# Kernel optimization log

Hardware: AMD Instinct MI355X
Metric: run time of the kernel (lower is better)

The kernel has to match this reference:

```python
import jax, jax.numpy as jnp
import numpy as np

N_ENT = 50000
N_REL = 16
D_E = 64
D_R = 64
D_OUT = 32
N_EDGE = 1000000


def setup_inputs() -> dict:
    key = jax.random.key(0)
    ks = jax.random.split(key, 8)
    # 0.1 scale keeps tanh / softmax in a realistic (non-saturated) range,
    # mimicking trained embedding magnitudes.
    entity_table = jax.random.normal(ks[0], (N_ENT, D_E), dtype=jnp.float32) * 0.1
    relation_table = jax.random.normal(ks[1], (N_REL, D_R), dtype=jnp.float32) * 0.1
    W_R = jax.random.normal(ks[2], (N_REL, D_E, D_R), dtype=jnp.float32) * (1.0 / np.sqrt(D_E))
    W1 = jax.random.normal(ks[3], (D_E, D_OUT), dtype=jnp.float32) * (1.0 / np.sqrt(D_E))
    b1 = jnp.zeros((D_OUT,), dtype=jnp.float32)
    W2 = jax.random.normal(ks[4], (D_E, D_OUT), dtype=jnp.float32) * (1.0 / np.sqrt(D_E))
    b2 = jnp.zeros((D_OUT,), dtype=jnp.float32)
    src = jax.random.randint(ks[5], (N_EDGE,), 0, N_ENT, dtype=jnp.int32)
    dst = jax.random.randint(ks[6], (N_EDGE,), 0, N_ENT, dtype=jnp.int32)
    etype = jax.random.randint(ks[7], (N_EDGE,), 0, N_REL, dtype=jnp.int32)
    return {"entity_table": entity_table, "relation_table": relation_table,
            "W_R": W_R, "W1": W1, "b1": b1, "W2": W2, "b2": b2,
            "src": src, "dst": dst, "etype": etype}


def reference(entity_table, relation_table, W_R, W1, b1, W2, b2, src, dst, etype):
    """KGAT calc_att (per-relation edge attention + edge softmax) followed by
    one bi-interaction Aggregator layer (dropout = identity, eval mode)."""
    n_nodes = entity_table.shape[0]
    # Per-relation projection of all node embeddings (grouped GEMM form of the
    # per-relation loop in compute_attention): [R, N, d_r]
    proj = jnp.einsum('nd,rde->rne', entity_table, W_R)
    r_mul_h = proj[etype, src]            # [E, d_r]  h W_r per edge
    r_mul_t = proj[etype, dst]            # [E, d_r]  t W_r per edge
    r_e = relation_table[etype]           # [E, d_r]
    # att = (h W_r) . tanh(t W_r + r)
    att = jnp.sum(r_mul_h * jnp.tanh(r_mul_t + r_e), axis=-1)  # [E]
    # edge softmax grouped by destination node
    att_max = jax.ops.segment_max(att, dst, num_segments=n_nodes)     # [N]
    ex = jnp.exp(att - att_max[dst])
    denom = jax.ops.segment_sum(ex, dst, num_segments=n_nodes)        # [N]
    a = ex / denom[dst]                                               # [E]
    # u_mul_e + sum: N_h[v] = sum_{(u->v)} a_e * node[u]
    msg = a[:, None] * entity_table[src]                              # [E, d]
    N_h = jax.ops.segment_sum(msg, dst, num_segments=n_nodes)         # [N, d]
    node = entity_table
    # bi-interaction aggregator (LeakyReLU slope 0.01, torch default)
    out1 = jax.nn.leaky_relu((node + N_h) @ W1 + b1)
    out2 = jax.nn.leaky_relu((node * N_h) @ W2 + b2)
    return out1 + out2
```

## Files before the change

kernel.cpp:

```cpp
#include <hip/hip_runtime.h>
#include <math.h>

#define NREL 16
#define DE 64
#define DOUT 32
#define NPART 16
#define TQ 392

typedef __attribute__((ext_vector_type(8))) short bf16x8;
typedef __attribute__((ext_vector_type(16))) float f32x16;
typedef __attribute__((ext_vector_type(2))) float f32x2;

__device__ __forceinline__ short f2bf(float f) {
    unsigned u = __builtin_bit_cast(unsigned, f);
    unsigned r = (u + 0x7FFFu + ((u >> 16) & 1u)) >> 16;
    return (short)r;
}
__device__ __forceinline__ unsigned char f2fp8(float f) {
    int p = __builtin_amdgcn_cvt_pk_fp8_f32(f, f, 0, false);
    return (unsigned char)(p & 0xff);
}
__device__ __forceinline__ float tanh_fast(float x) {
    float e = __expf(2.0f * x);
    return fmaf(-2.0f, __builtin_amdgcn_rcpf(e + 1.0f), 1.0f);
}
__device__ __forceinline__ void fp8x8_to_f32(uint2 u, float* f) {
    f32x2 a0 = __builtin_amdgcn_cvt_pk_f32_fp8(u.x, false);
    f32x2 a1 = __builtin_amdgcn_cvt_pk_f32_fp8(u.x, true);
    f32x2 a2 = __builtin_amdgcn_cvt_pk_f32_fp8(u.y, false);
    f32x2 a3 = __builtin_amdgcn_cvt_pk_f32_fp8(u.y, true);
    f[0] = a0[0]; f[1] = a0[1]; f[2] = a1[0]; f[3] = a1[1];
    f[4] = a2[0]; f[5] = a2[1]; f[6] = a3[0]; f[7] = a3[1];
}

__global__ __launch_bounds__(256) void prep_kernel(const float* __restrict__ ent,
                                                   short* __restrict__ entbf,
                                                   unsigned char* __restrict__ entf8,
                                                   int eTot,
                                                   const float* __restrict__ WR,
                                                   short* __restrict__ Wbf,
                                                   short* __restrict__ WTbf,
                                                   const int* __restrict__ dst,
                                                   int* __restrict__ counts,
                                                   int E, int psz,
                                                   int eB, int wB) {
    int b = blockIdx.x;
    if (b < eB) {
        int i = b * 256 + threadIdx.x;
        if (i < eTot) {
            float f = ent[i];
            entbf[i] = f2bf(f);
            entf8[i] = f2fp8(f);
        }
    } else if (b < eB + wB) {
        int i = (b - eB) * 256 + threadIdx.x;
        int r = i >> 12, k = (i >> 6) & 63, j = i & 63;
        short w = f2bf(WR[i]);
        Wbf[i] = w;
        WTbf[(r << 12) + (j << 6) + k] = w;
    } else {
        int hb = b - eB - wB;
        int part = hb & (NPART - 1);
        int i = (hb / NPART) * 256 + threadIdx.x;
        if (i < E) {
            int d = dst[i];
            if (d >= part * psz && d < (part + 1) * psz)
                atomicAdd(&counts[d], 1);
        }
    }
}

__global__ __launch_bounds__(256) void blocksum_kernel(const int* __restrict__ counts,
                                                       int* __restrict__ blockSums, int n) {
    __shared__ int wsum[4];
    int i = blockIdx.x * 256 + threadIdx.x;
    int v = (i < n) ? counts[i] : 0;
#pragma unroll
    for (int off = 1; off < 64; off <<= 1) v += __shfl_xor(v, off);
    if ((threadIdx.x & 63) == 0) wsum[threadIdx.x >> 6] = v;
    __syncthreads();
    if (threadIdx.x == 0)
        blockSums[blockIdx.x] = wsum[0] + wsum[1] + wsum[2] + wsum[3];
}

__global__ __launch_bounds__(1024) void blockscan_kernel(int* __restrict__ blockSums, int nb) {
    __shared__ int lds[1024];
    int t = threadIdx.x;
    int v = (t < nb) ? blockSums[t] : 0;
    lds[t] = v;
    __syncthreads();
    for (int off = 1; off < 1024; off <<= 1) {
        int u = (t >= off) ? lds[t - off] : 0;
        __syncthreads();
        lds[t] += u;
        __syncthreads();
    }
    if (t < nb) blockSums[t] = (t == 0) ? 0 : lds[t - 1];
}

__global__ __launch_bounds__(256) void scanout_kernel(const int* __restrict__ counts,
                                                      const int* __restrict__ blockSums,
                                                      int* __restrict__ offsets,
                                                      int* __restrict__ cursor, int n) {
    __shared__ int wsum[4];
    int t = threadIdx.x;
    int i = blockIdx.x * 256 + t;
    int lane = t & 63;
    int w = t >> 6;
    int v = (i < n) ? counts[i] : 0;
    int incl = v;
#pragma unroll
    for (int off = 1; off < 64; off <<= 1) {
        int u = __shfl_up(incl, off);
        if (lane >= off) incl += u;
    }
    if (lane == 63) wsum[w] = incl;
    __syncthreads();
    int woff = 0;
#pragma unroll
    for (int j = 0; j < 4; ++j) if (j < w) woff += wsum[j];
    int excl = incl - v + woff + blockSums[blockIdx.x];
    if (i < n) { offsets[i] = excl; cursor[i] = excl; }
    if (i == n - 1) offsets[n] = excl + v;
}

__global__ __launch_bounds__(256) void scatter_kernel(const int* __restrict__ dst,
                                                      const int* __restrict__ src,
                                                      const int* __restrict__ etype,
                                                      int* __restrict__ cursor,
                                                      int* __restrict__ pks,
                                                      int E, int psz) {
    int part = blockIdx.x & (NPART - 1);
    int i = (blockIdx.x / NPART) * 256 + threadIdx.x;
    if (i < E) {
        int d = dst[i];
        if (d >= part * psz && d < (part + 1) * psz) {
            int pos = atomicAdd(&cursor[d], 1);
            pks[pos] = (src[i] << 4) | etype[i];
        }
    }
}

__global__ __launch_bounds__(256) void projq_kernel(const short* __restrict__ entbf,
                                                    const float* __restrict__ rel,
                                                    const short* __restrict__ Wbf,
                                                    const short* __restrict__ WTbf,
                                                    unsigned char* __restrict__ Qf8,
                                                    int N) {
    __shared__ short Tl[4 * 2048];
    int lane = threadIdx.x & 63;
    int wid = threadIdx.x >> 6;
    int lin = blockIdx.x;
    int r = lin / TQ;
    int tq = lin - r * TQ;
    int m0 = (tq * 4 + wid) * 32;
    if (m0 >= N) return;
    int hi = lane >> 5;
    int lo = lane & 31;

    int arow = m0 + lo;
    if (arow >= N) arow = N - 1;
    const short* ap = entbf + ((size_t)arow << 6) + hi * 8;
    bf16x8 A[4];
#pragma unroll
    for (int kk = 0; kk < 4; ++kk) A[kk] = *(const bf16x8*)(ap + kk * 16);

    short* tb = Tl + wid * 2048;
    const short* wtb = WTbf + ((size_t)r << 12);
    const short* wb  = Wbf  + ((size_t)r << 12);

    f32x16 acc0 = {}, acc1 = {};
#pragma unroll
    for (int kk = 0; kk < 4; ++kk) {
        bf16x8 b0 = *(const bf16x8*)(wtb + lo * DE + kk * 16 + hi * 8);
        bf16x8 b1 = *(const bf16x8*)(wtb + (lo + 32) * DE + kk * 16 + hi * 8);
        acc0 = __builtin_amdgcn_mfma_f32_32x32x16_bf16(A[kk], b0, acc0, 0, 0, 0);
        acc1 = __builtin_amdgcn_mfma_f32_32x32x16_bf16(A[kk], b1, acc1, 0, 0, 0);
    }
    float rv0 = rel[r * DE + lo];
    float rv1 = rel[r * DE + 32 + lo];
#pragma unroll
    for (int i = 0; i < 16; ++i) {
        int row = (i & 3) + 8 * (i >> 2) + 4 * hi;
        int sw = (row & 7) << 3;
        tb[(row * DE + lo) ^ sw] = f2bf(tanh_fast(acc0[i] + rv0));
        tb[(row * DE + 32 + lo) ^ sw] = f2bf(tanh_fast(acc1[i] + rv1));
    }
    bf16x8 A2[4];
#pragma unroll
    for (int kk = 0; kk < 4; ++kk)
        A2[kk] = *(const bf16x8*)(tb + ((lo * DE + kk * 16 + hi * 8) ^ ((lo & 7) << 3)));

    f32x16 q0 = {}, q1 = {};
#pragma unroll
    for (int kk = 0; kk < 4; ++kk) {
        bf16x8 b0 = *(const bf16x8*)(wb + lo * DE + kk * 16 + hi * 8);
        bf16x8 b1 = *(const bf16x8*)(wb + (lo + 32) * DE + kk * 16 + hi * 8);
        q0 = __builtin_amdgcn_mfma_f32_32x32x16_bf16(A2[kk], b0, q0, 0, 0, 0);
        q1 = __builtin_amdgcn_mfma_f32_32x32x16_bf16(A2[kk], b1, q1, 0, 0, 0);
    }
    unsigned char* tb8 = (unsigned char*)tb;
#pragma unroll
    for (int i = 0; i < 16; ++i) {
        int row = (i & 3) + 8 * (i >> 2) + 4 * hi;
        tb8[row * DE + lo] = f2fp8(q0[i]);
        tb8[row * DE + 32 + lo] = f2fp8(q1[i]);
    }
#pragma unroll
    for (int p = 0; p < 4; ++p) {
        int row = p * 8 + (lane >> 3);
        int node = m0 + row;
        unsigned long long vq = *(const unsigned long long*)(tb8 + row * DE + (lane & 7) * 8);
        if (node < N)
            *(unsigned long long*)(Qf8 + (((size_t)r * N + node) << 6) + (lane & 7) * 8) = vq;
    }
}

__global__ __launch_bounds__(256) void agg_kernel(const float* __restrict__ ent,
                                                  const unsigned char* __restrict__ entf8,
                                                  const unsigned char* __restrict__ Qf8,
                                                  const int* __restrict__ offsets,
                                                  const int* __restrict__ pks,
                                                  const float* __restrict__ W1,
                                                  const float* __restrict__ b1,
                                                  const float* __restrict__ W2,
                                                  const float* __restrict__ b2,
                                                  float* __restrict__ out, int n) {
    __shared__ float xl[4][128];
    __shared__ unsigned char ql[4][NREL * DE];
    int lane = threadIdx.x & 63;
    int wid = threadIdx.x >> 6;
    int v = (blockIdx.x << 2) + wid;
    if (v >= n) return;
    int o0 = offsets[v], o1 = offsets[v + 1];
    int g = lane >> 3, gl = lane & 7;

    unsigned char* qw = &ql[wid][0];
#pragma unroll
    for (int pass = 0; pass < 4; ++pass) {
        int r = pass * 4 + (lane >> 4);
        int j4 = (lane & 15) * 4;
        unsigned qj = *(const unsigned*)(Qf8 + (((size_t)r * (unsigned)n + (unsigned)v) << 6) + j4);
        *(unsigned*)(&qw[(r << 6) + j4]) = qj;
    }

    float l = 0.f;
    float acc[8];
#pragma unroll
    for (int j = 0; j < 8; ++j) acc[j] = 0.f;

    int k0 = o0 + g;
    bool vv0 = k0 < o1;
    int pk0 = vv0 ? pks[k0] : 0;
    uint2 x0 = {};
    if (vv0) x0 = *(const uint2*)(entf8 + ((size_t)(pk0 >> 4) << 6) + gl * 8);
    int k1 = k0 + 8;
    bool vv1 = k1 < o1;
    int pk1 = vv1 ? pks[k1] : 0;
    uint2 x1 = {};
    if (vv1) x1 = *(const uint2*)(entf8 + ((size_t)(pk1 >> 4) << 6) + gl * 8);
    int k2 = k1 + 8;
    bool vv2 = k2 < o1;
    int pk2 = vv2 ? pks[k2] : 0;

    int iters = (o1 - o0 + 7) >> 3;
    for (int it = 0; it < iters; ++it) {
        uint2 x2 = {};
        if (vv2) x2 = *(const uint2*)(entf8 + ((size_t)(pk2 >> 4) << 6) + gl * 8);
        int k3 = k2 + 8;
        bool vv3 = k3 < o1;
        int pk3 = vv3 ? pks[k3] : 0;

        int rcur = pk0 & 15;
        uint2 qv = *(const uint2*)(&qw[(rcur << 6) + gl * 8]);
        float xf[8], qf[8];
        fp8x8_to_f32(x0, xf);
        fp8x8_to_f32(qv, qf);
        float d = 0.f;
#pragma unroll
        for (int j = 0; j < 8; ++j) d = fmaf(xf[j], qf[j], d);
        d += __shfl_xor(d, 1);
        d += __shfl_xor(d, 2);
        d += __shfl_xor(d, 4);
        float pe = vv0 ? __expf(d) : 0.f;
        l += pe;
#pragma unroll
        for (int j = 0; j < 8; ++j) acc[j] = fmaf(pe, xf[j], acc[j]);
        vv0 = vv1; x0 = x1; pk0 = pk1;
        vv1 = vv2; x1 = x2; pk1 = pk2;
        vv2 = vv3; pk2 = pk3; k2 = k3;
    }
#pragma unroll
    for (int off = 8; off < 64; off <<= 1) {
        l += __shfl_xor(l, off);
#pragma unroll
        for (int j = 0; j < 8; ++j) acc[j] += __shfl_xor(acc[j], off);
    }
    float* xw = &xl[wid][0];
    float invl = (l > 0.f) ? (1.0f / l) : 0.f;
    if (g == 0) {
#pragma unroll
        for (int j = 0; j < 8; ++j) xw[gl * 8 + j] = acc[j] * invl;
    }
    float node = ent[((size_t)v << 6) + lane];
    float Nh = xw[lane];
    float x1e = node + Nh;
    float x2e = node * Nh;
    xw[lane] = x1e;
    xw[64 + lane] = x2e;
    int j = lane & 31;
    const float* __restrict__ Wsel = (lane < 32) ? W1 : W2;
    float bias = (lane < 32) ? b1[j] : b2[j];
    const float* xb2 = xw + ((lane < 32) ? 0 : 64);
    float o = 0.f;
#pragma unroll 8
    for (int kk = 0; kk < DE; ++kk)
        o = fmaf(xb2[kk], Wsel[kk * DOUT + j], o);
    o += bias;
    float lr = (o > 0.f) ? o : 0.01f * o;
    float other = __shfl_xor(lr, 32);
    if (lane < 32) out[(size_t)v * DOUT + lane] = lr + other;
}

extern "C" void kernel_launch(void* const* d_in, const int* in_sizes, int n_in,
                              void* d_out, int out_size, void* d_ws, size_t ws_size,
                              hipStream_t stream) {
    const float* ent = (const float*)d_in[0];
    const float* rel = (const float*)d_in[1];
    const float* WR  = (const float*)d_in[2];
    const float* W1  = (const float*)d_in[3];
    const float* b1  = (const float*)d_in[4];
    const float* W2  = (const float*)d_in[5];
    const float* b2  = (const float*)d_in[6];
    const int* src   = (const int*)d_in[7];
    const int* dst   = (const int*)d_in[8];
    const int* ety   = (const int*)d_in[9];
    float* out       = (float*)d_out;

    const int E = in_sizes[7];
    const int N = in_sizes[0] / DE;
    const int NB = (N + 255) / 256;
    const int psz = (N + NPART - 1) / NPART;
    const int chunks = (E + 255) / 256;

    size_t qBytes  = (size_t)N * NREL * DE;
    size_t eElems  = (size_t)N * DE;
    size_t wElems  = (size_t)NREL * DE * DE;

    char* ws = (char*)d_ws;
    unsigned char* Qf8 = (unsigned char*)ws;
    short* entbf = (short*)(ws + qBytes);
    short* Wbf   = entbf + eElems;
    short* WTbf  = Wbf + wElems;
    unsigned char* entf8 = (unsigned char*)(WTbf + wElems);
    int* counts  = (int*)(entf8 + eElems);
    int* offsets = counts + N;
    int* cursor  = offsets + N + 1;
    int* pks     = cursor + N;
    int* bsums   = pks + E;
    size_t need  = (size_t)((char*)(bsums + NB) - ws);
    if (ws_size < need) return;

    const int eB = (int)((eElems + 255) / 256);
    const int wB = (int)(wElems / 256);

    hipMemsetAsync(counts, 0, (size_t)N * 4, stream);
    prep_kernel<<<eB + wB + chunks * NPART, 256, 0, stream>>>(
        ent, entbf, entf8, (int)eElems, WR, Wbf, WTbf, dst, counts, E, psz, eB, wB);
    blocksum_kernel<<<NB, 256, 0, stream>>>(counts, bsums, N);
    blockscan_kernel<<<1, 1024, 0, stream>>>(bsums, NB);
    scanout_kernel<<<NB, 256, 0, stream>>>(counts, bsums, offsets, cursor, N);
    scatter_kernel<<<chunks * NPART, 256, 0, stream>>>(dst, src, ety, cursor, pks, E, psz);
    projq_kernel<<<TQ * NREL, 256, 0, stream>>>(entbf, rel, Wbf, WTbf, Qf8, N);
    agg_kernel<<<(N + 3) / 4, 256, 0, stream>>>(ent, entf8, Qf8, offsets, pks,
                                                W1, b1, W2, b2, out, N);
}
```

Before: 227.9 us.

## Fuse per-relation projection into aggregation kernel via shared-memory Q tile

Merges the projection kernel and the aggregation kernel into one. Each block computes Q for its 32 destination nodes across all 16 relations into a 32KB shared-memory tile, then aggregates incoming edges for those nodes. This removes the global write and read of the N×16×64 FP8 Q buffer and one kernel launch. In exchange it uses much more LDS per block, which lowers occupancy, and it serialises the MFMA phase with the gather phase inside each block.

```diff
diff --git a/kernel.cpp b/kernel.cpp
--- a/kernel.cpp
+++ b/kernel.cpp
@@ -5,7 +5,6 @@
 #define DE 64
 #define DOUT 32
 #define NPART 16
-#define TQ 392
 
 typedef __attribute__((ext_vector_type(8))) short bf16x8;
 typedef __attribute__((ext_vector_type(16))) float f32x16;
@@ -141,185 +140,166 @@
     }
 }
 
-__global__ __launch_bounds__(256) void projq_kernel(const short* __restrict__ entbf,
-                                                    const float* __restrict__ rel,
-                                                    const short* __restrict__ Wbf,
-                                                    const short* __restrict__ WTbf,
-                                                    unsigned char* __restrict__ Qf8,
-                                                    int N) {
+__global__ __launch_bounds__(256) void projagg_kernel(const float* __restrict__ ent,
+                                                      const short* __restrict__ entbf,
+                                                      const unsigned char* __restrict__ entf8,
+                                                      const float* __restrict__ rel,
+                                                      const short* __restrict__ Wbf,
+                                                      const short* __restrict__ WTbf,
+                                                      const int* __restrict__ offsets,
+                                                      const int* __restrict__ pks,
+                                                      const float* __restrict__ W1,
+                                                      const float* __restrict__ b1,
+                                                      const float* __restrict__ W2,
+                                                      const float* __restrict__ b2,
+                                                      float* __restrict__ out, int N) {
     __shared__ short Tl[4 * 2048];
+    __shared__ unsigned char qtile[32][NREL][DE];
+    __shared__ float xl[4][128];
     int lane = threadIdx.x & 63;
     int wid = threadIdx.x >> 6;
-    int lin = blockIdx.x;
-    int r = lin / TQ;
-    int tq = lin - r * TQ;
-    int m0 = (tq * 4 + wid) * 32;
-    if (m0 >= N) return;
+    int m0 = blockIdx.x * 32;
     int hi = lane >> 5;
     int lo = lane & 31;
 
-    int arow = m0 + lo;
-    if (arow >= N) arow = N - 1;
-    const short* ap = entbf + ((size_t)arow << 6) + hi * 8;
-    bf16x8 A[4];
-#pragma unroll
-    for (int kk = 0; kk < 4; ++kk) A[kk] = *(const bf16x8*)(ap + kk * 16);
-
-    short* tb = Tl + wid * 2048;
-    const short* wtb = WTbf + ((size_t)r << 12);
-    const short* wb  = Wbf  + ((size_t)r << 12);
-
-    f32x16 acc0 = {}, acc1 = {};
-#pragma unroll
-    for (int kk = 0; kk < 4; ++kk) {
-        bf16x8 b0 = *(const bf16x8*)(wtb + lo * DE + kk * 16 + hi * 8);
-        bf16x8 b1 = *(const bf16x8*)(wtb + (lo + 32) * DE + kk * 16 + hi * 8);
-        acc0 = __builtin_amdgcn_mfma_f32_32x32x16_bf16(A[kk], b0, acc0, 0, 0, 0);
-        acc1 = __builtin_amdgcn_mfma_f32_32x32x16_bf16(A[kk], b1, acc1, 0, 0, 0);
-    }
-    float rv0 = rel[r * DE + lo];
-    float rv1 = rel[r * DE + 32 + lo];
-#pragma unroll
-    for (int i = 0; i < 16; ++i) {
-        int row = (i & 3) + 8 * (i >> 2) + 4 * hi;
-        int sw = (row & 7) << 3;
-        tb[(row * DE + lo) ^ sw] = f2bf(tanh_fast(acc0[i] + rv0));
-        tb[(row * DE + 32 + lo) ^ sw] = f2bf(tanh_fast(acc1[i] + rv1));
-    }
-    bf16x8 A2[4];
-#pragma unroll
-    for (int kk = 0; kk < 4; ++kk)
-        A2[kk] = *(const bf16x8*)(tb + ((lo * DE + kk * 16 + hi * 8) ^ ((lo & 7) << 3)));
-
-    f32x16 q0 = {}, q1 = {};
-#pragma unroll
-    for (int kk = 0; kk < 4; ++kk) {
-        bf16x8 b0 = *(const bf16x8*)(wb + lo * DE + kk * 16 + hi * 8);
-        bf16x8 b1 = *(const bf16x8*)(wb + (lo + 32) * DE + kk * 16 + hi * 8);
-        q0 = __builtin_amdgcn_mfma_f32_32x32x16_bf16(A2[kk], b0, q0, 0, 0, 0);
-        q1 = __builtin_amdgcn_mfma_f32_32x32x16_bf16(A2[kk], b1, q1, 0, 0, 0);
-    }
-    unsigned char* tb8 = (unsigned char*)tb;
-#pragma unroll
-    for (int i = 0; i < 16; ++i) {
-        int row = (i & 3) + 8 * (i >> 2) + 4 * hi;
-        tb8[row * DE + lo] = f2fp8(q0[i]);
-        tb8[row * DE + 32 + lo] = f2fp8(q1[i]);
-    }
-#pragma unroll
-    for (int p = 0; p < 4; ++p) {
-        int row = p * 8 + (lane >> 3);
-        int node = m0 + row;
-        unsigned long long vq = *(const unsigned long long*)(tb8 + row * DE + (lane & 7) * 8);
-        if (node < N)
-            *(unsigned long long*)(Qf8 + (((size_t)r * N + node) << 6) + (lane & 7) * 8) = vq;
-    }
-}
-
-__global__ __launch_bounds__(256) void agg_kernel(const float* __restrict__ ent,
-                                                  const unsigned char* __restrict__ entf8,
-                                                  const unsigned char* __restrict__ Qf8,
-                                                  const int* __restrict__ offsets,
-                                                  const int* __restrict__ pks,
-                                                  const float* __restrict__ W1,
-                                                  const float* __restrict__ b1,
-                                                  const float* __restrict__ W2,
-                                                  const float* __restrict__ b2,
-                                                  float* __restrict__ out, int n) {
-    __shared__ float xl[4][128];
-    __shared__ unsigned char ql[4][NREL * DE];
-    int lane = threadIdx.x & 63;
-    int wid = threadIdx.x >> 6;
-    int v = (blockIdx.x << 2) + wid;
-    if (v >= n) return;
-    int o0 = offsets[v], o1 = offsets[v + 1];
+    {
+        int arow = m0 + lo;
+        if (arow >= N) arow = N - 1;
+        const short* ap = entbf + ((size_t)arow << 6) + hi * 8;
+        bf16x8 A[4];
+#pragma unroll
+        for (int kk = 0; kk < 4; ++kk) A[kk] = *(const bf16x8*)(ap + kk * 16);
+
+        short* tb = Tl + wid * 2048;
+        for (int rr = 0; rr < 4; ++rr) {
+            int r = wid * 4 + rr;
+            const short* wtb = WTbf + ((size_t)r << 12);
+            const short* wb  = Wbf  + ((size_t)r << 12);
+
+            f32x16 acc0 = {}, acc1 = {};
+#pragma unroll
+            for (int kk = 0; kk < 4; ++kk) {
+                bf16x8 b0 = *(const bf16x8*)(wtb + lo * DE + kk * 16 + hi * 8);
+                bf16x8 b1 = *(const bf16x8*)(wtb + (lo + 32) * DE + kk * 16 + hi * 8);
+                acc0 = __builtin_amdgcn_mfma_f32_32x32x16_bf16(A[kk], b0, acc0, 0, 0, 0);
+                acc1 = __builtin_amdgcn_mfma_f32_32x32x16_bf16(A[kk], b1, acc1, 0, 0, 0);
+            }
+            float rv0 = rel[r * DE + lo];
+            float rv1 = rel[r * DE + 32 + lo];
+#pragma unroll
+            for (int i = 0; i < 16; ++i) {
+                int row = (i & 3) + 8 * (i >> 2) + 4 * hi;
+                int sw = (row & 7) << 3;
+                tb[(row * DE + lo) ^ sw] = f2bf(tanh_fast(acc0[i] + rv0));
+                tb[(row * DE + 32 + lo) ^ sw] = f2bf(tanh_fast(acc1[i] + rv1));
+            }
+            bf16x8 A2[4];
+#pragma unroll
+            for (int kk = 0; kk < 4; ++kk)
+                A2[kk] = *(const bf16x8*)(tb + ((lo * DE + kk * 16 + hi * 8) ^ ((lo & 7) << 3)));
+
+            f32x16 q0 = {}, q1 = {};
+#pragma unroll
+            for (int kk = 0; kk < 4; ++kk) {
+                bf16x8 b0 = *(const bf16x8*)(wb + lo * DE + kk * 16 + hi * 8);
+                bf16x8 b1 = *(const bf16x8*)(wb + (lo + 32) * DE + kk * 16 + hi * 8);
+                q0 = __builtin_amdgcn_mfma_f32_32x32x16_bf16(A2[kk], b0, q0, 0, 0, 0);
+                q1 = __builtin_amdgcn_mfma_f32_32x32x16_bf16(A2[kk], b1, q1, 0, 0, 0);
+            }
+#pragma unroll
+            for (int i = 0; i < 16; ++i) {
+                int row = (i & 3) + 8 * (i >> 2) + 4 * hi;
+                qtile[row][r][lo] = f2fp8(q0[i]);
+                qtile[row][r][32 + lo] = f2fp8(q1[i]);
+            }
+        }
+    }
+    __syncthreads();
+
     int g = lane >> 3, gl = lane & 7;
-
-    unsigned char* qw = &ql[wid][0];
-#pragma unroll
-    for (int pass = 0; pass < 4; ++pass) {
-        int r = pass * 4 + (lane >> 4);
-        int j4 = (lane & 15) * 4;
-        unsigned qj = *(const unsigned*)(Qf8 + (((size_t)r * (unsigned)n + (unsigned)v) << 6) + j4);
-        *(unsigned*)(&qw[(r << 6) + j4]) = qj;
-    }
-
-    float l = 0.f;
-    float acc[8];
-#pragma unroll
-    for (int j = 0; j < 8; ++j) acc[j] = 0.f;
-
-    int k0 = o0 + g;
-    bool vv0 = k0 < o1;
-    int pk0 = vv0 ? pks[k0] : 0;
-    uint2 x0 = {};
-    if (vv0) x0 = *(const uint2*)(entf8 + ((size_t)(pk0 >> 4) << 6) + gl * 8);
-    int k1 = k0 + 8;
-    bool vv1 = k1 < o1;
-    int pk1 = vv1 ? pks[k1] : 0;
-    uint2 x1 = {};
-    if (vv1) x1 = *(const uint2*)(entf8 + ((size_t)(pk1 >> 4) << 6) + gl * 8);
-    int k2 = k1 + 8;
-    bool vv2 = k2 < o1;
-    int pk2 = vv2 ? pks[k2] : 0;
-
-    int iters = (o1 - o0 + 7) >> 3;
-    for (int it = 0; it < iters; ++it) {
-        uint2 x2 = {};
-        if (vv2) x2 = *(const uint2*)(entf8 + ((size_t)(pk2 >> 4) << 6) + gl * 8);
-        int k3 = k2 + 8;
-        bool vv3 = k3 < o1;
-        int pk3 = vv3 ? pks[k3] : 0;
-
-        int rcur = pk0 & 15;
-        uint2 qv = *(const uint2*)(&qw[(rcur << 6) + gl * 8]);
-        float xf[8], qf[8];
-        fp8x8_to_f32(x0, xf);
-        fp8x8_to_f32(qv, qf);
-        float d = 0.f;
-#pragma unroll
-        for (int j = 0; j < 8; ++j) d = fmaf(xf[j], qf[j], d);
-        d += __shfl_xor(d, 1);
-        d += __shfl_xor(d, 2);
-        d += __shfl_xor(d, 4);
-        float pe = vv0 ? __expf(d) : 0.f;
-        l += pe;
-#pragma unroll
-        for (int j = 0; j < 8; ++j) acc[j] = fmaf(pe, xf[j], acc[j]);
-        vv0 = vv1; x0 = x1; pk0 = pk1;
-        vv1 = vv2; x1 = x2; pk1 = pk2;
-        vv2 = vv3; pk2 = pk3; k2 = k3;
-    }
-#pragma unroll
-    for (int off = 8; off < 64; off <<= 1) {
-        l += __shfl_xor(l, off);
-#pragma unroll
-        for (int j = 0; j < 8; ++j) acc[j] += __shfl_xor(acc[j], off);
-    }
-    float* xw = &xl[wid][0];
-    float invl = (l > 0.f) ? (1.0f / l) : 0.f;
-    if (g == 0) {
-#pragma unroll
-        for (int j = 0; j < 8; ++j) xw[gl * 8 + j] = acc[j] * invl;
-    }
-    float node = ent[((size_t)v << 6) + lane];
-    float Nh = xw[lane];
-    float x1e = node + Nh;
-    float x2e = node * Nh;
-    xw[lane] = x1e;
-    xw[64 + lane] = x2e;
-    int j = lane & 31;
-    const float* __restrict__ Wsel = (lane < 32) ? W1 : W2;
-    float bias = (lane < 32) ? b1[j] : b2[j];
-    const float* xb2 = xw + ((lane < 32) ? 0 : 64);
-    float o = 0.f;
+    for (int nl = 0; nl < 8; ++nl) {
+        int vl = wid * 8 + nl;
+        int v = m0 + vl;
+        if (v >= N) break;
+        int o0 = offsets[v], o1 = offsets[v + 1];
+
+        float l = 0.f;
+        float acc[8];
+#pragma unroll
+        for (int j = 0; j < 8; ++j) acc[j] = 0.f;
+
+        int k0 = o0 + g;
+        bool vv0 = k0 < o1;
+        int pk0 = vv0 ? pks[k0] : 0;
+        uint2 x0 = {};
+        if (vv0) x0 = *(const uint2*)(entf8 + ((size_t)(pk0 >> 4) << 6) + gl * 8);
+        int k1 = k0 + 8;
+        bool vv1 = k1 < o1;
+        int pk1 = vv1 ? pks[k1] : 0;
+        uint2 x1 = {};
+        if (vv1) x1 = *(const uint2*)(entf8 + ((size_t)(pk1 >> 4) << 6) + gl * 8);
+        int k2 = k1 + 8;
+        bool vv2 = k2 < o1;
+        int pk2 = vv2 ? pks[k2] : 0;
+
+        int iters = (o1 - o0 + 7) >> 3;
+        for (int it = 0; it < iters; ++it) {
+            uint2 x2 = {};
+            if (vv2) x2 = *(const uint2*)(entf8 + ((size_t)(pk2 >> 4) << 6) + gl * 8);
+            int k3 = k2 + 8;
+            bool vv3 = k3 < o1;
+            int pk3 = vv3 ? pks[k3] : 0;
+
+            int rcur = pk0 & 15;
+            uint2 qv = *(const uint2*)(&qtile[vl][rcur][gl * 8]);
+            float xf[8], qf[8];
+            fp8x8_to_f32(x0, xf);
+            fp8x8_to_f32(qv, qf);
+            float d = 0.f;
+#pragma unroll
+            for (int j = 0; j < 8; ++j) d = fmaf(xf[j], qf[j], d);
+            d += __shfl_xor(d, 1);
+            d += __shfl_xor(d, 2);
+            d += __shfl_xor(d, 4);
+            float pe = vv0 ? __expf(d) : 0.f;
+            l += pe;
+#pragma unroll
+            for (int j = 0; j < 8; ++j) acc[j] = fmaf(pe, xf[j], acc[j]);
+            vv0 = vv1; x0 = x1; pk0 = pk1;
+            vv1 = vv2; x1 = x2; pk1 = pk2;
+            vv2 = vv3; pk2 = pk3; k2 = k3;
+        }
+#pragma unroll
+        for (int off = 8; off < 64; off <<= 1) {
+            l += __shfl_xor(l, off);
+#pragma unroll
+            for (int j = 0; j < 8; ++j) acc[j] += __shfl_xor(acc[j], off);
+        }
+        float* xw = &xl[wid][0];
+        float invl = (l > 0.f) ? (1.0f / l) : 0.f;
+        if (g == 0) {
+#pragma unroll
+            for (int j = 0; j < 8; ++j) xw[gl * 8 + j] = acc[j] * invl;
+        }
+        float node = ent[((size_t)v << 6) + lane];
+        float Nh = xw[lane];
+        float x1e = node + Nh;
+        float x2e = node * Nh;
+        xw[lane] = x1e;
+        xw[64 + lane] = x2e;
+        int j = lane & 31;
+        const float* __restrict__ Wsel = (lane < 32) ? W1 : W2;
+        float bias = (lane < 32) ? b1[j] : b2[j];
+        const float* xb2 = xw + ((lane < 32) ? 0 : 64);
+        float o = 0.f;
 #pragma unroll 8
-    for (int kk = 0; kk < DE; ++kk)
-        o = fmaf(xb2[kk], Wsel[kk * DOUT + j], o);
-    o += bias;
-    float lr = (o > 0.f) ? o : 0.01f * o;
-    float other = __shfl_xor(lr, 32);
-    if (lane < 32) out[(size_t)v * DOUT + lane] = lr + other;
+        for (int kk = 0; kk < DE; ++kk)
+            o = fmaf(xb2[kk], Wsel[kk * DOUT + j], o);
+        o += bias;
+        float lr = (o > 0.f) ? o : 0.01f * o;
+        float other = __shfl_xor(lr, 32);
+        if (lane < 32) out[(size_t)v * DOUT + lane] = lr + other;
+    }
 }
 
 extern "C" void kernel_launch(void* const* d_in, const int* in_sizes, int n_in,
@@ -343,13 +323,11 @@
     const int psz = (N + NPART - 1) / NPART;
     const int chunks = (E + 255) / 256;
 
-    size_t qBytes  = (size_t)N * NREL * DE;
     size_t eElems  = (size_t)N * DE;
     size_t wElems  = (size_t)NREL * DE * DE;
 
     char* ws = (char*)d_ws;
-    unsigned char* Qf8 = (unsigned char*)ws;
-    short* entbf = (short*)(ws + qBytes);
+    short* entbf = (short*)ws;
     short* Wbf   = entbf + eElems;
     short* WTbf  = Wbf + wElems;
     unsigned char* entf8 = (unsigned char*)(WTbf + wElems);
@@ -371,7 +349,6 @@
     blockscan_kernel<<<1, 1024, 0, stream>>>(bsums, NB);
     scanout_kernel<<<NB, 256, 0, stream>>>(counts, bsums, offsets, cursor, N);
     scatter_kernel<<<chunks * NPART, 256, 0, stream>>>(dst, src, ety, cursor, pks, E, psz);
-    projq_kernel<<<TQ * NREL, 256, 0, stream>>>(entbf, rel, Wbf, WTbf, Qf8, N);
-    agg_kernel<<<(N + 3) / 4, 256, 0, stream>>>(ent, entf8, Qf8, offsets, pks,
-                                                W1, b1, W2, b2, out, N);
-}
+    projagg_kernel<<<(N + 31) / 32, 256, 0, stream>>>(
+        ent, entbf, entf8, rel, Wbf, WTbf, offsets, pks, W1, b1, W2, b2, out, N);
+}
```

Result: slower. 282.2 us (+23.8%).

## Pre-bucket edges by destination partition with wave ballots before histogram and scatter

Applied to the files above, without the earlier changes.

The old histogram and scatter passes each launched 16 partition-filtered blocks per edge chunk, so dst, src and etype were reread 16 times. A new bucket kernel reads each edge once, compacts it into per-wave, per-partition staging slots using ballot and popcount, and records per-slot counts. The histogram and scatter kernels then read only their partition's staged entries, keeping atomics localized per partition. The cost is a large extra staging buffer, NW*16*64 uint2 entries of which most are empty, an added kernel launch, and sparse reads of that buffer.

```diff
diff --git a/kernel.cpp b/kernel.cpp
--- a/kernel.cpp
+++ b/kernel.cpp
@@ -40,10 +40,7 @@
                                                    const float* __restrict__ WR,
                                                    short* __restrict__ Wbf,
                                                    short* __restrict__ WTbf,
-                                                   const int* __restrict__ dst,
-                                                   int* __restrict__ counts,
-                                                   int E, int psz,
-                                                   int eB, int wB) {
+                                                   int eB) {
     int b = blockIdx.x;
     if (b < eB) {
         int i = b * 256 + threadIdx.x;
@@ -52,20 +49,56 @@
             entbf[i] = f2bf(f);
             entf8[i] = f2fp8(f);
         }
-    } else if (b < eB + wB) {
+    } else {
         int i = (b - eB) * 256 + threadIdx.x;
         int r = i >> 12, k = (i >> 6) & 63, j = i & 63;
         short w = f2bf(WR[i]);
         Wbf[i] = w;
         WTbf[(r << 12) + (j << 6) + k] = w;
-    } else {
-        int hb = b - eB - wB;
-        int part = hb & (NPART - 1);
-        int i = (hb / NPART) * 256 + threadIdx.x;
-        if (i < E) {
-            int d = dst[i];
-            if (d >= part * psz && d < (part + 1) * psz)
-                atomicAdd(&counts[d], 1);
+    }
+}
+
+__global__ __launch_bounds__(256) void bucket_kernel(const int* __restrict__ dst,
+                                                     const int* __restrict__ src,
+                                                     const int* __restrict__ etype,
+                                                     uint2* __restrict__ staging,
+                                                     int* __restrict__ cnts,
+                                                     int E, int psz, int NW) {
+    int wid = threadIdx.x >> 6, lane = threadIdx.x & 63;
+    int w = blockIdx.x * 4 + wid;
+    if (w >= NW) return;
+    int base = w * 64 + lane;
+    bool act = base < E;
+    int d = act ? dst[base] : 0;
+    int pk = act ? ((src[base] << 4) | etype[base]) : 0;
+    int dp = act ? (d / psz) : -1;
+#pragma unroll
+    for (int p = 0; p < NPART; ++p) {
+        unsigned long long mask = __ballot(dp == p);
+        int cnt = __popcll(mask);
+        if (dp == p) {
+            int mypos = __popcll(mask & ((1ull << lane) - 1ull));
+            staging[((size_t)w * NPART + p) * 64 + mypos] =
+                make_uint2((unsigned)pk, (unsigned)d);
+        }
+        if (lane == 0) cnts[w * NPART + p] = cnt;
+    }
+}
+
+__global__ __launch_bounds__(256) void hist2_kernel(const uint2* __restrict__ staging,
+                                                    const int* __restrict__ cnts,
+                                                    int* __restrict__ counts,
+                                                    int NW, int W) {
+    int p = blockIdx.x & (NPART - 1);
+    int g = blockIdx.x / NPART;
+    int wid = threadIdx.x >> 6, lane = threadIdx.x & 63;
+    int start = g * W;
+    int end = min(start + W, NW);
+    for (int wb = start + wid; wb < end; wb += 4) {
+        int cnt = cnts[wb * NPART + p];
+        if (lane < cnt) {
+            uint2 e = staging[((size_t)wb * NPART + p) * 64 + lane];
+            atomicAdd(&counts[e.y], 1);
         }
     }
 }
@@ -124,19 +157,22 @@
     if (i == n - 1) offsets[n] = excl + v;
 }
 
-__global__ __launch_bounds__(256) void scatter_kernel(const int* __restrict__ dst,
-                                                      const int* __restrict__ src,
-                                                      const int* __restrict__ etype,
-                                                      int* __restrict__ cursor,
-                                                      int* __restrict__ pks,
-                                                      int E, int psz) {
-    int part = blockIdx.x & (NPART - 1);
-    int i = (blockIdx.x / NPART) * 256 + threadIdx.x;
-    if (i < E) {
-        int d = dst[i];
-        if (d >= part * psz && d < (part + 1) * psz) {
-            int pos = atomicAdd(&cursor[d], 1);
-            pks[pos] = (src[i] << 4) | etype[i];
+__global__ __launch_bounds__(256) void scatter2_kernel(const uint2* __restrict__ staging,
+                                                       const int* __restrict__ cnts,
+                                                       int* __restrict__ cursor,
+                                                       int* __restrict__ pks,
+                                                       int NW, int W) {
+    int p = blockIdx.x & (NPART - 1);
+    int g = blockIdx.x / NPART;
+    int wid = threadIdx.x >> 6, lane = threadIdx.x & 63;
+    int start = g * W;
+    int end = min(start + W, NW);
+    for (int wb = start + wid; wb < end; wb += 4) {
+        int cnt = cnts[wb * NPART + p];
+        if (lane < cnt) {
+            uint2 e = staging[((size_t)wb * NPART + p) * 64 + lane];
+            int pos = atomicAdd(&cursor[e.y], 1);
+            pks[pos] = (int)e.x;
         }
     }
 }
@@ -341,15 +377,20 @@
     const int N = in_sizes[0] / DE;
     const int NB = (N + 255) / 256;
     const int psz = (N + NPART - 1) / NPART;
-    const int chunks = (E + 255) / 256;
+    const int NW = (E + 63) / 64;
+    const int G = 256;
+    const int W = (NW + G - 1) / G;
 
     size_t qBytes  = (size_t)N * NREL * DE;
     size_t eElems  = (size_t)N * DE;
     size_t wElems  = (size_t)NREL * DE * DE;
+    size_t stElems = (size_t)NW * NPART * 64;
 
     char* ws = (char*)d_ws;
-    unsigned char* Qf8 = (unsigned char*)ws;
-    short* entbf = (short*)(ws + qBytes);
+    uint2* staging = (uint2*)ws;
+    int* cnts      = (int*)(staging + stElems);
+    unsigned char* Qf8 = (unsigned char*)(cnts + (size_t)NW * NPART);
+    short* entbf = (short*)(Qf8 + qBytes);
     short* Wbf   = entbf + eElems;
     short* WTbf  = Wbf + wElems;
     unsigned char* entf8 = (unsigned char*)(WTbf + wElems);
@@ -365,12 +406,15 @@
     const int wB = (int)(wElems / 256);
 
     hipMemsetAsync(counts, 0, (size_t)N * 4, stream);
-    prep_kernel<<<eB + wB + chunks * NPART, 256, 0, stream>>>(
-        ent, entbf, entf8, (int)eElems, WR, Wbf, WTbf, dst, counts, E, psz, eB, wB);
+    prep_kernel<<<eB + wB, 256, 0, stream>>>(ent, entbf, entf8, (int)eElems,
+                                             WR, Wbf, WTbf, eB);
+    bucket_kernel<<<(NW + 3) / 4, 256, 0, stream>>>(dst, src, ety, staging, cnts,
+                                                    E, psz, NW);
+    hist2_kernel<<<G * NPART, 256, 0, stream>>>(staging, cnts, counts, NW, W);
     blocksum_kernel<<<NB, 256, 0, stream>>>(counts, bsums, N);
     blockscan_kernel<<<1, 1024, 0, stream>>>(bsums, NB);
     scanout_kernel<<<NB, 256, 0, stream>>>(counts, bsums, offsets, cursor, N);
-    scatter_kernel<<<chunks * NPART, 256, 0, stream>>>(dst, src, ety, cursor, pks, E, psz);
+    scatter2_kernel<<<G * NPART, 256, 0, stream>>>(staging, cnts, cursor, pks, NW, W);
     projq_kernel<<<TQ * NREL, 256, 0, stream>>>(entbf, rel, Wbf, WTbf, Qf8, N);
     agg_kernel<<<(N + 3) / 4, 256, 0, stream>>>(ent, entf8, Qf8, offsets, pks,
                                                 W1, b1, W2, b2, out, N);
```

Result: slower. 243.9 us (+7.0%).
